# Kernel optimization log

Measured on AMD Instinct MI355X. Metric: run time of the kernel, lower is better.

## Reference

```python
import jax, jax.numpy as jnp
import numpy as np

VOCAB, EMB, HID = 128, 512, 1024
B, T = 256, 256


def setup_inputs() -> dict:
    key = jax.random.key(0)
    ks = jax.random.split(key, 12)
    sc_e = 1.0 / np.sqrt(EMB)
    sc_h = 1.0 / np.sqrt(HID)
    u = lambda k, shape, s: jax.random.uniform(k, shape, jnp.float32, -s, s)
    return {
        "tokens": jax.random.randint(ks[0], (B, T), 0, VOCAB),
        "emb": jax.random.normal(ks[1], (VOCAB, EMB), jnp.float32),
        # layer 0: input size EMB
        "W_ih0": u(ks[2], (HID, EMB), sc_h), "W_hh0": u(ks[3], (HID, HID), sc_h),
        "b_ih0": u(ks[4], (HID,), sc_h), "b_hh0": u(ks[5], (HID,), sc_h),
        # layer 1: input size HID
        "W_ih1": u(ks[6], (HID, HID), sc_h), "W_hh1": u(ks[7], (HID, HID), sc_h),
        "b_ih1": u(ks[8], (HID,), sc_h), "b_hh1": u(ks[9], (HID,), sc_h),
        # output head
        "W_out": u(ks[10], (VOCAB, HID), sc_h), "b_out": u(ks[11], (VOCAB,), sc_h),
    }


def _rnn_layer(x, W_ih, W_hh, b_ih, b_hh):
    # x: [B, T, I] -> [B, T, H]; precompute the input projection as one big GEMM
    pre = jnp.einsum('bti,hi->bth', x, W_ih) + b_ih  # [B, T, H]
    h0 = jnp.zeros((x.shape[0], W_hh.shape[0]), x.dtype)

    def step(h, p):
        h = jnp.tanh(p + h @ W_hh.T + b_hh)
        return h, h

    _, ys = jax.lax.scan(step, h0, jnp.swapaxes(pre, 0, 1))  # ys: [T, B, H]
    return jnp.swapaxes(ys, 0, 1)


def reference(tokens, emb, W_ih0, W_hh0, b_ih0, b_hh0,
              W_ih1, W_hh1, b_ih1, b_hh1, W_out, b_out):
    x = emb[tokens]                                    # [B, T, EMB]
    x = _rnn_layer(x, W_ih0, W_hh0, b_ih0, b_hh0)      # [B, T, HID]
    x = _rnn_layer(x, W_ih1, W_hh1, b_ih1, b_hh1)      # [B, T, HID]
    return x[:, -1, :] @ W_out.T + b_out               # [B, VOCAB]
```

## Files before the change

### kernel.cpp

```cpp
#include <hip/hip_runtime.h>

typedef _Float16 f16x8 __attribute__((ext_vector_type(8)));
typedef float f32x4 __attribute__((ext_vector_type(4)));

#define VOCAB 128
#define EMB 512
#define HID 1024
#define BATCH 256
#define TSEQ 256
#define SLOT (BATCH * HID)

#define CTR0_B 0
#define CTRG_B 1024
#define CTR1_B 2048
#define H0_B   4096
#define H1_B   (H0_B + 4 * SLOT * 2)
#define PRE1_B (H1_B + 4 * SLOT * 2)
#define PROJ_B (PRE1_B + 4 * SLOT * 4)
#define WIMG_B (PROJ_B + VOCAB * HID * 4)

#define LOADX4(dst, p) asm volatile("global_load_dwordx4 %0, %1, off sc0 sc1" : "=v"(dst) : "v"(p))
#define LOADD(dst, p)  asm volatile("global_load_dword %0, %1, off sc0 sc1" : "=v"(dst) : "v"(p))
#define STOREX4(p, v)  asm volatile("global_store_dwordx4 %0, %1, off sc0 sc1" :: "v"(p), "v"(v) : "memory")
#define WAITV(n) do { asm volatile("s_waitcnt vmcnt(" #n ")" ::: "memory"); \
                      __builtin_amdgcn_sched_barrier(0); } while (0)

__device__ __forceinline__ f32x4 mfma16(f16x8 a, f16x8 b, f32x4 c) {
    return __builtin_amdgcn_mfma_f32_16x16x32_f16(a, b, c, 0, 0, 0);
}

__device__ __forceinline__ void spin64(unsigned int* p) {
    while (__hip_atomic_load(p, __ATOMIC_RELAXED, __HIP_MEMORY_SCOPE_AGENT) < 64u)
        __builtin_amdgcn_s_sleep(1);
}

__global__ __launch_bounds__(256) void pack_w(const float* __restrict__ W,
                                              _Float16* __restrict__ img) {
    int i = blockIdx.x * 256 + threadIdx.x;
    if (i >= HID * 128) return;
    const int n = i >> 7;
    const int c = i & 127;
    const int cb = n >> 5;
    const int col = n & 31;
    const int nf = col >> 4, ar = col & 15;
    const int kc = c >> 2, g = c & 3;
    const float* src = W + (size_t)n * HID + c * 8;
    float4 u0 = *(const float4*)src;
    float4 u1 = *(const float4*)(src + 4);
    float uf[8] = {u0.x, u0.y, u0.z, u0.w, u1.x, u1.y, u1.z, u1.w};
    f16x8 hi, lo;
    #pragma unroll
    for (int j = 0; j < 8; ++j) {
        _Float16 h = (_Float16)uf[j];
        hi[j] = h;
        lo[j] = (_Float16)(uf[j] - (float)h);
    }
    const size_t base = (size_t)cb * 65536 + (size_t)kc * 2048 +
                        (size_t)nf * 512 + (size_t)g * 128 + (size_t)ar * 8;
    *(f16x8*)(img + base)        = hi;
    *(f16x8*)(img + base + 1024) = lo;
}

__global__ __launch_bounds__(256) void proj_k(const float* __restrict__ emb,
                                              const float* __restrict__ Wih0,
                                              const float* __restrict__ b_ih0,
                                              float* __restrict__ PROJ) {
    int o = blockIdx.x * 256 + threadIdx.x;
    if (o >= VOCAB * HID) return;
    const int v = o >> 10, n = o & (HID - 1);
    const float* er = emb + (size_t)v * EMB;
    const float* wr = Wih0 + (size_t)n * EMB;
    float acc = 0.f;
    #pragma unroll 4
    for (int k = 0; k < EMB; k += 4) {
        float4 e = *(const float4*)(er + k);
        float4 w = *(const float4*)(wr + k);
        acc += e.x * w.x + e.y * w.y + e.z * w.z + e.w * w.w;
    }
    PROJ[o] = acc + b_ih0[n];
}

#define ISSUE4(B0, B1, KCB) do { \
    const _Float16* q0_ = pr0 + (KCB) * 32; \
    const _Float16* q1_ = pr1 + (KCB) * 32; \
    LOADX4(B0[0], q0_);      LOADX4(B0[1], q0_ + 32); \
    LOADX4(B0[2], q0_ + 64); LOADX4(B0[3], q0_ + 96); \
    LOADX4(B1[0], q1_);      LOADX4(B1[1], q1_ + 32); \
    LOADX4(B1[2], q1_ + 64); LOADX4(B1[3], q1_ + 96); \
} while (0)

#define KC1(KC, AV0, AV1) do { \
    const _Float16* sb_ = simg + (KC) * 2048 + lane * 8; \
    f16x8 bh0_ = *(const f16x8*)sb_; \
    f16x8 bh1_ = *(const f16x8*)(sb_ + 512); \
    f16x8 bl0_ = *(const f16x8*)(sb_ + 1024); \
    f16x8 bl1_ = *(const f16x8*)(sb_ + 1536); \
    a00 = mfma16(AV0, bh0_, a00); a01 = mfma16(AV0, bh1_, a01); \
    a10 = mfma16(AV1, bh0_, a10); a11 = mfma16(AV1, bh1_, a11); \
    a00 = mfma16(AV0, bl0_, a00); a01 = mfma16(AV0, bl1_, a01); \
    a10 = mfma16(AV1, bl0_, a10); a11 = mfma16(AV1, bl1_, a11); \
} while (0)

#define KC4(KB, CB0, CB1) do { \
    KC1((KB) + 0, CB0[0], CB1[0]); \
    KC1((KB) + 1, CB0[1], CB1[1]); \
    KC1((KB) + 2, CB0[2], CB1[2]); \
    KC1((KB) + 3, CB0[3], CB1[3]); \
} while (0)

__global__ __launch_bounds__(256, 1) void rnn_run(
    const int* __restrict__ tokens,
    const float* __restrict__ b_hh0, const float* __restrict__ b_ih1,
    const float* __restrict__ b_hh1, char* __restrict__ ws)
{
    __shared__ _Float16 simg[65536];
    __shared__ __align__(16) char stageb[4][4096];

    unsigned int* ctr0 = (unsigned int*)(ws + CTR0_B);
    unsigned int* ctrG = (unsigned int*)(ws + CTRG_B);
    unsigned int* ctr1 = (unsigned int*)(ws + CTR1_B);
    _Float16* h0 = (_Float16*)(ws + H0_B);
    _Float16* h1 = (_Float16*)(ws + H1_B);
    float* pre1 = (float*)(ws + PRE1_B);
    const float* PROJ = (const float*)(ws + PROJ_B);
    const _Float16* wimg = (const _Float16*)(ws + WIMG_B);

    const int tid = threadIdx.x, lane = tid & 63, wv = tid >> 6;
    const int blk = blockIdx.x;
    const int role = blk >> 6;
    const int sub = blk & 63;
    const int cb = sub & 31, rg = sub >> 5;
    const int n0 = cb * 32;

    {
        const _Float16* gi = wimg + (size_t)(role * 32 + cb) * 65536;
        for (int i = tid; i < 8192; i += 256)
            *(f16x8*)&simg[(size_t)i * 8] = *(const f16x8*)&gi[(size_t)i * 8];
    }
    __syncthreads();

    const int ar = lane & 15;
    const int g16 = lane >> 4;
    const int rbase = rg * 128 + wv * 32;
    const int er0 = rbase + g16 * 4;

    const float* bias = (role == 0) ? b_hh0 : (role == 1) ? b_ih1 : b_hh1;
    const float b0 = bias[n0 + ar];
    const float b1 = bias[n0 + 16 + ar];
    unsigned int* ctr_pub = (role == 0) ? ctr0 : (role == 1) ? ctrG : ctr1;

    for (int st = 0; st < TSEQ; ++st) {
        if (tid == 0) {
            if (role == 0) {
                if (st)      spin64(ctr0 + st - 1);
                if (st >= 4) spin64(ctrG + st - 4);
            } else if (role == 1) {
                spin64(ctr0 + st);
                if (st >= 4) spin64(ctr1 + st - 4);
            } else {
                spin64(ctrG + st);
                if (st)      spin64(ctr1 + st - 1);
            }
        }
        __syncthreads();

        const _Float16* A = (role == 0) ? h0 + (size_t)((st + 3) & 3) * SLOT
                          : (role == 1) ? h0 + (size_t)(st & 3) * SLOT
                                        : h1 + (size_t)((st + 3) & 3) * SLOT;
        const _Float16* pr0 = A + (size_t)(rbase + ar) * HID + g16 * 8;
        const _Float16* pr1 = pr0 + 16 * HID;

        f32x4 a00 = {}, a01 = {}, a10 = {}, a11 = {};
        f16x8 ca0[4], ca1[4], cb0[4], cb1[4];

        __builtin_amdgcn_sched_barrier(0);
        ISSUE4(ca0, ca1, 0);
        #pragma unroll
        for (int k8 = 0; k8 < 4; ++k8) {
            const int kb = k8 * 8;
            ISSUE4(cb0, cb1, kb + 4);
            WAITV(8);
            KC4(kb, ca0, ca1);
            if (k8 < 3) {
                ISSUE4(ca0, ca1, kb + 8);
                WAITV(8);
            } else {
                WAITV(0);
            }
            KC4(kb + 4, cb0, cb1);
        }
        __builtin_amdgcn_sched_barrier(0);

        if (role == 0) {
            _Float16* sg = (_Float16*)stageb[wv];
            _Float16* O = h0 + (size_t)(st & 3) * SLOT;
            #pragma unroll
            for (int mf = 0; mf < 2; ++mf) {
                #pragma unroll
                for (int r = 0; r < 4; ++r) {
                    const int rr = er0 + mf * 16 + r;
                    const int trow = g16 * 4 + mf * 16 + r;
                    const int tok = tokens[rr * TSEQ + st];
                    const float* pr = PROJ + (size_t)tok * HID + n0;
                    const float v0 = (mf ? a10[r] : a00[r]) + pr[ar] + b0;
                    const float v1 = (mf ? a11[r] : a01[r]) + pr[16 + ar] + b1;
                    sg[trow * 32 + ar]      = (_Float16)tanhf(v0);
                    sg[trow * 32 + 16 + ar] = (_Float16)tanhf(v1);
                }
            }
            __syncthreads();
            #pragma unroll
            for (int j = 0; j < 2; ++j) {
                const int trow = j * 16 + (lane >> 2);
                f32x4 sv = *(const f32x4*)((const char*)sg + trow * 64 + (lane & 3) * 16);
                STOREX4(O + (size_t)(rbase + trow) * HID + n0 + (lane & 3) * 8, sv);
            }
        } else if (role == 1) {
            float* sg = (float*)stageb[wv];
            float* O = pre1 + (size_t)(st & 3) * SLOT;
            #pragma unroll
            for (int mf = 0; mf < 2; ++mf) {
                #pragma unroll
                for (int r = 0; r < 4; ++r) {
                    const int trow = g16 * 4 + mf * 16 + r;
                    sg[trow * 32 + ar]      = (mf ? a10[r] : a00[r]) + b0;
                    sg[trow * 32 + 16 + ar] = (mf ? a11[r] : a01[r]) + b1;
                }
            }
            __syncthreads();
            #pragma unroll
            for (int i = 0; i < 4; ++i) {
                const int trow = i * 8 + (lane >> 3);
                f32x4 sv = *(const f32x4*)((const char*)sg + trow * 128 + (lane & 7) * 16);
                STOREX4(O + (size_t)(rbase + trow) * HID + n0 + (lane & 7) * 4, sv);
            }
        } else {
            const float* P = pre1 + (size_t)(st & 3) * SLOT;
            float pv0[8], pv1[8];
            #pragma unroll
            for (int mf = 0; mf < 2; ++mf) {
                #pragma unroll
                for (int r = 0; r < 4; ++r) {
                    const int rr = er0 + mf * 16 + r;
                    LOADD(pv0[mf * 4 + r], P + (size_t)rr * HID + n0 + ar);
                    LOADD(pv1[mf * 4 + r], P + (size_t)rr * HID + n0 + 16 + ar);
                }
            }
            WAITV(0);
            _Float16* sg = (_Float16*)stageb[wv];
            _Float16* O = h1 + (size_t)(st & 3) * SLOT;
            #pragma unroll
            for (int mf = 0; mf < 2; ++mf) {
                #pragma unroll
                for (int r = 0; r < 4; ++r) {
                    const int trow = g16 * 4 + mf * 16 + r;
                    const float v0 = (mf ? a10[r] : a00[r]) + pv0[mf * 4 + r] + b0;
                    const float v1 = (mf ? a11[r] : a01[r]) + pv1[mf * 4 + r] + b1;
                    sg[trow * 32 + ar]      = (_Float16)tanhf(v0);
                    sg[trow * 32 + 16 + ar] = (_Float16)tanhf(v1);
                }
            }
            __syncthreads();
            #pragma unroll
            for (int j = 0; j < 2; ++j) {
                const int trow = j * 16 + (lane >> 2);
                f32x4 sv = *(const f32x4*)((const char*)sg + trow * 64 + (lane & 3) * 16);
                STOREX4(O + (size_t)(rbase + trow) * HID + n0 + (lane & 3) * 8, sv);
            }
        }

        asm volatile("s_waitcnt vmcnt(0)" ::: "memory");
        __syncthreads();
        if (tid == 0)
            __hip_atomic_fetch_add(ctr_pub + st, 1u, __ATOMIC_RELAXED,
                                   __HIP_MEMORY_SCOPE_AGENT);
    }
}

__global__ __launch_bounds__(256) void head2(const _Float16* __restrict__ h1last,
                                             const float* __restrict__ Wout,
                                             const float* __restrict__ b_out,
                                             float* __restrict__ out) {
    const int idx = blockIdx.x * 256 + threadIdx.x;
    const int m = idx >> 7, n = idx & 127;
    const _Float16* hr = h1last + (size_t)m * HID;
    const float* wr = Wout + (size_t)n * HID;
    float acc = 0.f;
    #pragma unroll 4
    for (int k = 0; k < HID; k += 8) {
        f16x8 hv = *(const f16x8*)(hr + k);
        float4 w0 = *(const float4*)(wr + k);
        float4 w1 = *(const float4*)(wr + k + 4);
        acc += (float)hv[0] * w0.x + (float)hv[1] * w0.y +
               (float)hv[2] * w0.z + (float)hv[3] * w0.w +
               (float)hv[4] * w1.x + (float)hv[5] * w1.y +
               (float)hv[6] * w1.z + (float)hv[7] * w1.w;
    }
    out[idx] = acc + b_out[n];
}

extern "C" void kernel_launch(void* const* d_in, const int* in_sizes, int n_in,
                              void* d_out, int out_size, void* d_ws, size_t ws_size,
                              hipStream_t stream) {
    const int*   tokens = (const int*)  d_in[0];
    const float* emb    = (const float*)d_in[1];
    const float* W_ih0  = (const float*)d_in[2];
    const float* W_hh0  = (const float*)d_in[3];
    const float* b_ih0  = (const float*)d_in[4];
    const float* b_hh0  = (const float*)d_in[5];
    const float* W_ih1  = (const float*)d_in[6];
    const float* W_hh1  = (const float*)d_in[7];
    const float* b_ih1  = (const float*)d_in[8];
    const float* b_hh1  = (const float*)d_in[9];
    const float* W_out  = (const float*)d_in[10];
    const float* b_out  = (const float*)d_in[11];
    float* out = (float*)d_out;

    char* ws = (char*)d_ws;
    _Float16* wimg = (_Float16*)(ws + WIMG_B);
    float* PROJ = (float*)(ws + PROJ_B);

    (void)hipMemsetAsync(ws + CTR0_B, 0, 4096, stream);
    (void)hipMemsetAsync(ws + H0_B + (size_t)3 * SLOT * 2, 0, (size_t)SLOT * 2, stream);
    (void)hipMemsetAsync(ws + H1_B + (size_t)3 * SLOT * 2, 0, (size_t)SLOT * 2, stream);

    pack_w<<<512, 256, 0, stream>>>(W_hh0, wimg);
    pack_w<<<512, 256, 0, stream>>>(W_ih1, wimg + (size_t)32 * 65536);
    pack_w<<<512, 256, 0, stream>>>(W_hh1, wimg + (size_t)64 * 65536);
    proj_k<<<512, 256, 0, stream>>>(emb, W_ih0, b_ih0, PROJ);

    rnn_run<<<192, 256, 0, stream>>>(tokens, b_hh0, b_ih1, b_hh1, ws);

    head2<<<128, 256, 0, stream>>>((const _Float16*)(ws + H1_B) + (size_t)3 * SLOT,
                                   W_out, b_out, out);
}
```

Measured before the change: 4.640 ms.

## Split step counters per row group, defer WAR waits, deepen load pipeline

Step counters are now kept per batch row group, so each block waits on the 32 blocks sharing its rows instead of all 64. This lets the two halves of the batch advance independently. The write-after-read waits on the ring slots (ctrG/ctr1 four steps back) move to after the MFMA loop so they overlap the matvec. The role-2 pre1 loads are issued before the GEMM, and the k-loop keeps four outstanding load groups instead of two. The risks are higher register pressure and subtle ordering errors in the cross-block protocol.

```diff
diff --git a/kernel.cpp b/kernel.cpp
--- a/kernel.cpp
+++ b/kernel.cpp
@@ -11,9 +11,9 @@
 #define SLOT (BATCH * HID)
 
 #define CTR0_B 0
-#define CTRG_B 1024
-#define CTR1_B 2048
-#define H0_B   4096
+#define CTRG_B 2048
+#define CTR1_B 4096
+#define H0_B   8192
 #define H1_B   (H0_B + 4 * SLOT * 2)
 #define PRE1_B (H1_B + 4 * SLOT * 2)
 #define PROJ_B (PRE1_B + 4 * SLOT * 4)
@@ -29,8 +29,8 @@
     return __builtin_amdgcn_mfma_f32_16x16x32_f16(a, b, c, 0, 0, 0);
 }
 
-__device__ __forceinline__ void spin64(unsigned int* p) {
-    while (__hip_atomic_load(p, __ATOMIC_RELAXED, __HIP_MEMORY_SCOPE_AGENT) < 64u)
+__device__ __forceinline__ void spin32(unsigned int* p) {
+    while (__hip_atomic_load(p, __ATOMIC_RELAXED, __HIP_MEMORY_SCOPE_AGENT) < 32u)
         __builtin_amdgcn_s_sleep(1);
 }
 
@@ -116,9 +116,6 @@
     __shared__ _Float16 simg[65536];
     __shared__ __align__(16) char stageb[4][4096];
 
-    unsigned int* ctr0 = (unsigned int*)(ws + CTR0_B);
-    unsigned int* ctrG = (unsigned int*)(ws + CTRG_B);
-    unsigned int* ctr1 = (unsigned int*)(ws + CTR1_B);
     _Float16* h0 = (_Float16*)(ws + H0_B);
     _Float16* h1 = (_Float16*)(ws + H1_B);
     float* pre1 = (float*)(ws + PRE1_B);
@@ -132,6 +129,11 @@
     const int cb = sub & 31, rg = sub >> 5;
     const int n0 = cb * 32;
 
+    unsigned int* c0 = (unsigned int*)(ws + CTR0_B) + (rg << 8);
+    unsigned int* cG = (unsigned int*)(ws + CTRG_B) + (rg << 8);
+    unsigned int* c1 = (unsigned int*)(ws + CTR1_B) + (rg << 8);
+    unsigned int* ctr_pub = (role == 0) ? c0 : (role == 1) ? cG : c1;
+
     {
         const _Float16* gi = wimg + (size_t)(role * 32 + cb) * 65536;
         for (int i = tid; i < 8192; i += 256)
@@ -147,19 +149,16 @@
     const float* bias = (role == 0) ? b_hh0 : (role == 1) ? b_ih1 : b_hh1;
     const float b0 = bias[n0 + ar];
     const float b1 = bias[n0 + 16 + ar];
-    unsigned int* ctr_pub = (role == 0) ? ctr0 : (role == 1) ? ctrG : ctr1;
 
     for (int st = 0; st < TSEQ; ++st) {
         if (tid == 0) {
             if (role == 0) {
-                if (st)      spin64(ctr0 + st - 1);
-                if (st >= 4) spin64(ctrG + st - 4);
+                if (st) spin32(c0 + st - 1);
             } else if (role == 1) {
-                spin64(ctr0 + st);
-                if (st >= 4) spin64(ctr1 + st - 4);
+                spin32(c0 + st);
             } else {
-                spin64(ctrG + st);
-                if (st)      spin64(ctr1 + st - 1);
+                spin32(cG + st);
+                if (st) spin32(c1 + st - 1);
             }
         }
         __syncthreads();
@@ -171,25 +170,44 @@
         const _Float16* pr1 = pr0 + 16 * HID;
 
         f32x4 a00 = {}, a01 = {}, a10 = {}, a11 = {};
-        f16x8 ca0[4], ca1[4], cb0[4], cb1[4];
+        f16x8 cA0[4], cA1[4], cB0[4], cB1[4], cC0[4], cC1[4], cD0[4], cD1[4];
+        float pv0[8], pv1[8];
 
         __builtin_amdgcn_sched_barrier(0);
-        ISSUE4(ca0, ca1, 0);
-        #pragma unroll
-        for (int k8 = 0; k8 < 4; ++k8) {
-            const int kb = k8 * 8;
-            ISSUE4(cb0, cb1, kb + 4);
-            WAITV(8);
-            KC4(kb, ca0, ca1);
-            if (k8 < 3) {
-                ISSUE4(ca0, ca1, kb + 8);
-                WAITV(8);
-            } else {
-                WAITV(0);
-            }
-            KC4(kb + 4, cb0, cb1);
+        if (role == 2) {
+            const float* P = pre1 + (size_t)(st & 3) * SLOT;
+            #pragma unroll
+            for (int mf = 0; mf < 2; ++mf) {
+                #pragma unroll
+                for (int r = 0; r < 4; ++r) {
+                    const int rr = er0 + mf * 16 + r;
+                    LOADD(pv0[mf * 4 + r], P + (size_t)rr * HID + n0 + ar);
+                    LOADD(pv1[mf * 4 + r], P + (size_t)rr * HID + n0 + 16 + ar);
+                }
+            }
         }
+        ISSUE4(cA0, cA1, 0);
+        ISSUE4(cB0, cB1, 4);
+        ISSUE4(cC0, cC1, 8);
+        ISSUE4(cD0, cD1, 12);
+        WAITV(24); KC4(0,  cA0, cA1); ISSUE4(cA0, cA1, 16);
+        WAITV(24); KC4(4,  cB0, cB1); ISSUE4(cB0, cB1, 20);
+        WAITV(24); KC4(8,  cC0, cC1); ISSUE4(cC0, cC1, 24);
+        WAITV(24); KC4(12, cD0, cD1); ISSUE4(cD0, cD1, 28);
+        WAITV(24); KC4(16, cA0, cA1);
+        WAITV(16); KC4(20, cB0, cB1);
+        WAITV(8);  KC4(24, cC0, cC1);
+        WAITV(0);  KC4(28, cD0, cD1);
         __builtin_amdgcn_sched_barrier(0);
+
+        if (tid == 0) {
+            if (role == 0) {
+                if (st >= 4) spin32(cG + st - 4);
+            } else if (role == 1) {
+                if (st >= 4) spin32(c1 + st - 4);
+            }
+        }
+        __syncthreads();
 
         if (role == 0) {
             _Float16* sg = (_Float16*)stageb[wv];
@@ -235,18 +253,6 @@
                 STOREX4(O + (size_t)(rbase + trow) * HID + n0 + (lane & 7) * 4, sv);
             }
         } else {
-            const float* P = pre1 + (size_t)(st & 3) * SLOT;
-            float pv0[8], pv1[8];
-            #pragma unroll
-            for (int mf = 0; mf < 2; ++mf) {
-                #pragma unroll
-                for (int r = 0; r < 4; ++r) {
-                    const int rr = er0 + mf * 16 + r;
-                    LOADD(pv0[mf * 4 + r], P + (size_t)rr * HID + n0 + ar);
-                    LOADD(pv1[mf * 4 + r], P + (size_t)rr * HID + n0 + 16 + ar);
-                }
-            }
-            WAITV(0);
             _Float16* sg = (_Float16*)stageb[wv];
             _Float16* O = h1 + (size_t)(st & 3) * SLOT;
             #pragma unroll
@@ -320,7 +326,7 @@
     _Float16* wimg = (_Float16*)(ws + WIMG_B);
     float* PROJ = (float*)(ws + PROJ_B);
 
-    (void)hipMemsetAsync(ws + CTR0_B, 0, 4096, stream);
+    (void)hipMemsetAsync(ws + CTR0_B, 0, 8192, stream);
     (void)hipMemsetAsync(ws + H0_B + (size_t)3 * SLOT * 2, 0, (size_t)SLOT * 2, stream);
     (void)hipMemsetAsync(ws + H1_B + (size_t)3 * SLOT * 2, 0, (size_t)SLOT * 2, stream);
 
```

Result: faster. 4.335 ms (-6.6%).
